# Kernel optimization log

Hardware: AMD Instinct MI355X
Metric: run time of the kernel (lower is better)

Reference implementation:

```python
import jax, jax.numpy as jnp
import numpy as np

NEG_INF = -1e38


def _wkv_scan(time_decay, time_first, key, value):
    # key, value: [B, S, D]; time_decay/time_first: [D]
    B, S, D = key.shape
    w = -jnp.exp(time_decay)  # decay applied additively in log-space

    def step(carry, kv):
        num, den, mx = carry
        k, v = kv  # [B, D]
        # output with current token boosted by time_first
        m_out = jnp.maximum(mx, k + time_first)
        e1 = jnp.exp(mx - m_out)
        e2 = jnp.exp(k + time_first - m_out)
        out = (e1 * num + e2 * v) / (e1 * den + e2)
        # state update with decay
        m_new = jnp.maximum(mx + w, k)
        e1 = jnp.exp(mx + w - m_new)
        e2 = jnp.exp(k - m_new)
        return (e1 * num + e2 * v, e1 * den + e2, m_new), out

    init = (jnp.zeros((B, D), jnp.float32),
            jnp.zeros((B, D), jnp.float32),
            jnp.full((B, D), NEG_INF, jnp.float32))
    kv = (jnp.moveaxis(key, 1, 0), jnp.moveaxis(value, 1, 0))  # [S, B, D]
    _, out = jax.lax.scan(step, init, kv)
    return jnp.moveaxis(out, 0, 1)  # [B, S, D]


def setup_inputs() -> dict:
    key = jax.random.key(0)
    ks = jax.random.split(key, 10)
    B, S, H = 4, 2048, 2048
    D = H  # attention_hidden_size
    return {
        "hidden": jax.random.normal(ks[0], (B, S, H), jnp.float32),
        "time_decay": jax.random.normal(ks[1], (D,), jnp.float32),
        "time_first": jax.random.normal(ks[2], (D,), jnp.float32),
        "time_mix_key": jax.random.uniform(ks[3], (1, 1, H), jnp.float32),
        "time_mix_value": jax.random.uniform(ks[4], (1, 1, H), jnp.float32),
        "time_mix_receptance": jax.random.uniform(ks[5], (1, 1, H), jnp.float32),
        "Wk": jax.random.normal(ks[6], (D, H), jnp.float32) / np.sqrt(H),  # torch Linear weight [out, in]
        "Wv": jax.random.normal(ks[7], (D, H), jnp.float32) / np.sqrt(H),
        "Wr": jax.random.normal(ks[8], (D, H), jnp.float32) / np.sqrt(H),
        "Wo": jax.random.normal(ks[9], (H, D), jnp.float32) / np.sqrt(D),
    }


def reference(hidden, time_decay, time_first, time_mix_key, time_mix_value,
              time_mix_receptance, Wk, Wv, Wr, Wo):
    # time_shift: prepend a zero timestep, drop the last (ZeroPad2d((0,0,1,-1)))
    shifted = jnp.pad(hidden, ((0, 0), (1, 0), (0, 0)))[:, :-1]
    xk = hidden * time_mix_key + shifted * (1.0 - time_mix_key)
    xv = hidden * time_mix_value + shifted * (1.0 - time_mix_value)
    xr = hidden * time_mix_receptance + shifted * (1.0 - time_mix_receptance)
    k = jnp.einsum('bsh,dh->bsd', xk, Wk)
    v = jnp.einsum('bsh,dh->bsd', xv, Wv)
    r = jax.nn.sigmoid(jnp.einsum('bsh,dh->bsd', xr, Wr))
    rwkv = _wkv_scan(time_decay, time_first, k, v)
    return jnp.einsum('bsd,hd->bsh', r * rwkv, Wo)
```

## Files before the change

### kernel.cpp

```cpp
#include <hip/hip_runtime.h>


typedef __attribute__((ext_vector_type(8))) short s16x8;
typedef __attribute__((ext_vector_type(16))) float f32x16;

__device__ __forceinline__ unsigned short f2bf(float f) {
  union { float f; unsigned u; } v; v.f = f;
  unsigned r = v.u + 0x7fffu + ((v.u >> 16) & 1u);
  return (unsigned short)(r >> 16);
}
__device__ __forceinline__ float bf2f(unsigned short h) {
  union { unsigned u; float f; } v; v.u = ((unsigned)h) << 16; return v.f;
}
__device__ __forceinline__ void gload_lds16(const void* g, void* l) {
  __builtin_amdgcn_global_load_lds(
      (const __attribute__((address_space(1))) void*)g,
      (__attribute__((address_space(3))) void*)l, 16, 0, 0);
}


__global__ void conv_bf16(const float4* __restrict__ src, ushort4* __restrict__ dst, int n4) {
  int i = blockIdx.x * blockDim.x + threadIdx.x;
  if (i >= n4) return;
  float4 v = src[i];
  ushort4 o;
  o.x = f2bf(v.x); o.y = f2bf(v.y); o.z = f2bf(v.z); o.w = f2bf(v.w);
  dst[i] = o;
}


__global__ void prep_mix3(const float4* __restrict__ hidden,
                          const float4* __restrict__ tmk,
                          const float4* __restrict__ tmv,
                          const float4* __restrict__ tmr,
                          ushort4* __restrict__ xk, ushort4* __restrict__ xv,
                          ushort4* __restrict__ xr,
                          int S, int H4, long long total4) {
  long long i = (long long)blockIdx.x * blockDim.x + threadIdx.x;
  if (i >= total4) return;
  int h4 = (int)(i % H4);
  long long sb = i / H4;
  int s = (int)(sb % S);
  float4 cur = hidden[i];
  float4 prev = make_float4(0.f, 0.f, 0.f, 0.f);
  if (s > 0) prev = hidden[i - H4];
  float4 mk = tmk[h4], mv = tmv[h4], mr = tmr[h4];
  ushort4 ok, ov, orr;
  ok.x = f2bf(cur.x * mk.x + prev.x * (1.f - mk.x));
  ok.y = f2bf(cur.y * mk.y + prev.y * (1.f - mk.y));
  ok.z = f2bf(cur.z * mk.z + prev.z * (1.f - mk.z));
  ok.w = f2bf(cur.w * mk.w + prev.w * (1.f - mk.w));
  ov.x = f2bf(cur.x * mv.x + prev.x * (1.f - mv.x));
  ov.y = f2bf(cur.y * mv.y + prev.y * (1.f - mv.y));
  ov.z = f2bf(cur.z * mv.z + prev.z * (1.f - mv.z));
  ov.w = f2bf(cur.w * mv.w + prev.w * (1.f - mv.w));
  orr.x = f2bf(cur.x * mr.x + prev.x * (1.f - mr.x));
  orr.y = f2bf(cur.y * mr.y + prev.y * (1.f - mr.y));
  orr.z = f2bf(cur.z * mr.z + prev.z * (1.f - mr.z));
  orr.w = f2bf(cur.w * mr.w + prev.w * (1.f - mr.w));
  xk[i] = ok; xv[i] = ov; xr[i] = orr;
}


#define TM 128
#define TN 128
#define TK 32

template <int EPI>
__global__ __launch_bounds__(256) void gemm_bt(
    const unsigned short* __restrict__ A, const unsigned short* __restrict__ B,
    float* __restrict__ Cf, unsigned short* __restrict__ Cb,
    int M, int N, int K) {
  __shared__ unsigned short lA[2][TM * TK];
  __shared__ unsigned short lB[2][TN * TK];

  const int tid = threadIdx.x;
  const int wave = tid >> 6;
  const int lane = tid & 63;
  const int bm = blockIdx.x * TM;
  const int bn = blockIdx.y * TN;
  const int wm = (wave >> 1) * 64;
  const int wn = (wave & 1) * 64;
  const int lrow = lane & 31;
  const int lq = lane >> 5;

  f32x16 acc[2][2] = {};

  const int st_row0 = wave * 16 + (lane >> 2);
  const int st_row1 = (wave + 4) * 16 + (lane >> 2);
  const int st_c0 = (lane & 3) ^ ((st_row0 >> 1) & 3);
  const int st_c1 = (lane & 3) ^ ((st_row1 >> 1) & 3);
  const unsigned short* pA0 = A + (long long)(bm + st_row0) * K + st_c0 * 8;
  const unsigned short* pA1 = A + (long long)(bm + st_row1) * K + st_c1 * 8;
  const unsigned short* pB0 = B + (long long)(bn + st_row0) * K + st_c0 * 8;
  const unsigned short* pB1 = B + (long long)(bn + st_row1) * K + st_c1 * 8;

  int offA[2][2], offB[2][2];
#pragma unroll
  for (int t = 0; t < 2; ++t)
#pragma unroll
    for (int h = 0; h < 2; ++h) {
      int ar = wm + t * 32 + lrow;
      int br = wn + t * 32 + lrow;
      int c = h * 2 + lq;
      offA[t][h] = ar * TK + ((c ^ ((ar >> 1) & 3)) * 8);
      offB[t][h] = br * TK + ((c ^ ((br >> 1) & 3)) * 8);
    }

  gload_lds16(pA0, &lA[0][wave * 512]);
  gload_lds16(pA1, &lA[0][(wave + 4) * 512]);
  gload_lds16(pB0, &lB[0][wave * 512]);
  gload_lds16(pB1, &lB[0][(wave + 4) * 512]);
  pA0 += TK; pA1 += TK; pB0 += TK; pB1 += TK;

  int p = 0;
  for (int k0 = 0; k0 < K; k0 += TK) {
    __syncthreads();
    if (k0 + TK < K) {
      gload_lds16(pA0, &lA[p ^ 1][wave * 512]);
      gload_lds16(pA1, &lA[p ^ 1][(wave + 4) * 512]);
      gload_lds16(pB0, &lB[p ^ 1][wave * 512]);
      gload_lds16(pB1, &lB[p ^ 1][(wave + 4) * 512]);
      pA0 += TK; pA1 += TK; pB0 += TK; pB1 += TK;
    }

    s16x8 af[2][2], bfr[2][2];
#pragma unroll
    for (int t = 0; t < 2; ++t)
#pragma unroll
      for (int h = 0; h < 2; ++h) {
        af[t][h]  = *(const s16x8*)&lA[p][offA[t][h]];
        bfr[t][h] = *(const s16x8*)&lB[p][offB[t][h]];
      }
#pragma unroll
    for (int h = 0; h < 2; ++h)
#pragma unroll
      for (int mt = 0; mt < 2; ++mt)
#pragma unroll
        for (int nt = 0; nt < 2; ++nt)
          acc[mt][nt] = __builtin_amdgcn_mfma_f32_32x32x16_bf16(
              af[mt][h], bfr[nt][h], acc[mt][nt], 0, 0, 0);
    p ^= 1;
  }

#pragma unroll
  for (int mt = 0; mt < 2; ++mt)
#pragma unroll
    for (int nt = 0; nt < 2; ++nt)
#pragma unroll
      for (int r = 0; r < 16; ++r) {
        int row = bm + wm + mt * 32 + (r & 3) + 8 * (r >> 2) + 4 * lq;
        int col = bn + wn + nt * 32 + lrow;
        float v = acc[mt][nt][r];
        long long idx = (long long)row * N + col;
        if (EPI == 0) {
          Cf[idx] = v;
        } else if (EPI == 1) {
          float s = 1.f / (1.f + __expf(-v));
          Cb[idx] = f2bf(s);
        } else {
          Cb[idx] = f2bf(v);
        }
      }
}


#define NEG_INF_F (-1e38f)

__global__ void scan_phase1(const unsigned short* __restrict__ kb,
                            const unsigned short* __restrict__ vb,
                            const float* __restrict__ td,
                            float* __restrict__ locN, float* __restrict__ locD,
                            float* __restrict__ locM,
                            int S, int D, int C, int L) {
  int t = blockIdx.x * blockDim.x + threadIdx.x;
  int d = t % D;
  int c = (t / D) % C;
  int b = t / (D * C);
  float w = -__expf(td[d]);
  float num = 0.f, den = 0.f, m = NEG_INF_F;
  long long base = ((long long)(b * S + c * L)) * D + d;
  for (int i = 0; i < L; ++i) {
    float kk = bf2f(kb[base]);
    float vv = bf2f(vb[base]);
    base += D;
    float mn = fmaxf(m + w, kk);
    float e1 = __expf(m + w - mn);
    float e2 = __expf(kk - mn);
    num = e1 * num + e2 * vv;
    den = e1 * den + e2;
    m = mn;
  }
  int o = (b * C + c) * D + d;
  locN[o] = num; locD[o] = den; locM[o] = m;
}

__global__ void scan_phase2(const float* __restrict__ td,
                            const float* __restrict__ locN, const float* __restrict__ locD,
                            const float* __restrict__ locM,
                            float* __restrict__ inN, float* __restrict__ inD,
                            float* __restrict__ inM,
                            int Bc, int D, int C, int L) {
  int t = blockIdx.x * blockDim.x + threadIdx.x;
  if (t >= Bc * D) return;
  int d = t % D, b = t / D;
  float w = -__expf(td[d]);
  float Lw = (float)L * w;
  float num = 0.f, den = 0.f, m = NEG_INF_F;
  for (int c = 0; c < C; ++c) {
    int o = (b * C + c) * D + d;
    inN[o] = num; inD[o] = den; inM[o] = m;
    float sm = m + Lw;
    float lm = locM[o];
    float m2 = fmaxf(sm, lm);
    float e1 = __expf(sm - m2);
    float e2 = __expf(lm - m2);
    num = e1 * num + e2 * locN[o];
    den = e1 * den + e2 * locD[o];
    m = m2;
  }
}

__global__ void scan_phase3(const unsigned short* __restrict__ kb,
                            const unsigned short* __restrict__ vb,
                            const unsigned short* __restrict__ rb,
                            const float* __restrict__ td, const float* __restrict__ tfirst,
                            const float* __restrict__ inN, const float* __restrict__ inD,
                            const float* __restrict__ inM,
                            unsigned short* __restrict__ rr,
                            int S, int D, int C, int L) {
  int t = blockIdx.x * blockDim.x + threadIdx.x;
  int d = t % D;
  int c = (t / D) % C;
  int b = t / (D * C);
  float w = -__expf(td[d]);
  float tfd = tfirst[d];
  int o = (b * C + c) * D + d;
  float num = inN[o], den = inD[o], m = inM[o];
  long long base = ((long long)(b * S + c * L)) * D + d;
  for (int i = 0; i < L; ++i) {
    float kk = bf2f(kb[base]);
    float vv = bf2f(vb[base]);
    float rv = bf2f(rb[base]);
    float ktf = kk + tfd;
    float mo = fmaxf(m, ktf);
    float e1 = __expf(m - mo);
    float e2 = __expf(ktf - mo);
    float out = (e1 * num + e2 * vv) / (e1 * den + e2);
    rr[base] = f2bf(out * rv);
    float mn = fmaxf(m + w, kk);
    e1 = __expf(m + w - mn);
    e2 = __expf(kk - mn);
    num = e1 * num + e2 * vv;
    den = e1 * den + e2;
    m = mn;
    base += D;
  }
}


extern "C" void kernel_launch(void* const* d_in, const int* in_sizes, int n_in,
                              void* d_out, int out_size, void* d_ws, size_t ws_size,
                              hipStream_t stream) {
  const float* hidden = (const float*)d_in[0];
  const float* td  = (const float*)d_in[1];
  const float* tfi = (const float*)d_in[2];
  const float* tmk = (const float*)d_in[3];
  const float* tmv = (const float*)d_in[4];
  const float* tmr = (const float*)d_in[5];
  const float* Wk  = (const float*)d_in[6];
  const float* Wv  = (const float*)d_in[7];
  const float* Wr  = (const float*)d_in[8];
  const float* Wo  = (const float*)d_in[9];
  float* out = (float*)d_out;

  const int H = in_sizes[1];
  const int D = H;
  const long long BS = (long long)in_sizes[0] / H;
  const int S = 2048;
  const int B = (int)(BS / S);
  const int C = 32, L = S / C;

  char* ws = (char*)d_ws;
  const size_t MB = 1u << 20;
  unsigned short* W_b = (unsigned short*)(ws + 0 * MB);
  unsigned short* X   = (unsigned short*)(ws + 8 * MB);
  unsigned short* Y   = (unsigned short*)(ws + 40 * MB);
  unsigned short* Z   = (unsigned short*)(ws + 72 * MB);
  float* locN         = (float*)(ws + 104 * MB);
  float* locD         = (float*)(ws + 105 * MB);
  float* locM         = (float*)(ws + 106 * MB);
  float* inN          = (float*)(ws + 107 * MB);
  float* inD          = (float*)(ws + 108 * MB);
  float* inM          = (float*)(ws + 109 * MB);
  unsigned short* kb  = (unsigned short*)out;

  int n4w = H * H / 4;
  int cbk = (n4w + 255) / 256;
  long long total4 = BS * H / 4;
  int pbk = (int)((total4 + 255) / 256);
  dim3 g((unsigned)(BS / TM), (unsigned)(D / TN));

  prep_mix3<<<pbk, 256, 0, stream>>>((const float4*)hidden,
                                     (const float4*)tmk, (const float4*)tmv, (const float4*)tmr,
                                     (ushort4*)X, (ushort4*)Y, (ushort4*)Z, S, H / 4, total4);

  conv_bf16<<<cbk, 256, 0, stream>>>((const float4*)Wk, (ushort4*)W_b, n4w);
  gemm_bt<2><<<g, 256, 0, stream>>>(X, W_b, nullptr, kb, (int)BS, D, H);

  conv_bf16<<<cbk, 256, 0, stream>>>((const float4*)Wv, (ushort4*)W_b, n4w);
  gemm_bt<2><<<g, 256, 0, stream>>>(Y, W_b, nullptr, X, (int)BS, D, H);

  conv_bf16<<<cbk, 256, 0, stream>>>((const float4*)Wr, (ushort4*)W_b, n4w);
  gemm_bt<1><<<g, 256, 0, stream>>>(Z, W_b, nullptr, Y, (int)BS, D, H);

  int nscan = B * C * D;
  scan_phase1<<<nscan / 256, 256, 0, stream>>>(kb, X, td, locN, locD, locM, S, D, C, L);
  scan_phase2<<<(B * D + 255) / 256, 256, 0, stream>>>(td, locN, locD, locM, inN, inD, inM, B, D, C, L);
  scan_phase3<<<nscan / 256, 256, 0, stream>>>(kb, X, Y, td, tfi, inN, inD, inM, Z, S, D, C, L);

  conv_bf16<<<cbk, 256, 0, stream>>>((const float4*)Wo, (ushort4*)W_b, n4w);
  gemm_bt<0><<<g, 256, 0, stream>>>(Z, W_b, out, nullptr, (int)BS, H, D);
}
```

Baseline: 644.1 us.

## Enlarge GEMM tiles to 256x256 with 4-stage LDS pipeline and XCD-aware block remap

Rewrites the bf16 GEMM to use 256x256 output tiles computed by 512 threads, each wave owning a 128x64 sub-tile. Global-to-LDS loads run three stages ahead through a four-buffer ring, with explicit vmcnt waits and barriers replacing double buffering. Blocks are remapped so consecutive IDs spread across the eight XCDs, and MFMA sections raise wave priority. The goal is more data reuse per LDS load and better latency hiding, in exchange for 128KB of LDS per block, more registers, and fewer blocks (256) to fill the GPU.

```diff
diff --git a/kernel.cpp b/kernel.cpp
--- a/kernel.cpp
+++ b/kernel.cpp
@@ -62,89 +62,117 @@
 }
 
 
-#define TM 128
-#define TN 128
-#define TK 32
-
 template <int EPI>
-__global__ __launch_bounds__(256) void gemm_bt(
+__global__ __launch_bounds__(512) void gemm_bt(
     const unsigned short* __restrict__ A, const unsigned short* __restrict__ B,
     float* __restrict__ Cf, unsigned short* __restrict__ Cb,
     int M, int N, int K) {
-  __shared__ unsigned short lA[2][TM * TK];
-  __shared__ unsigned short lB[2][TN * TK];
+  __shared__ unsigned short lds[4][16384];
 
   const int tid = threadIdx.x;
   const int wave = tid >> 6;
   const int lane = tid & 63;
-  const int bm = blockIdx.x * TM;
-  const int bn = blockIdx.y * TN;
-  const int wm = (wave >> 1) * 64;
-  const int wn = (wave & 1) * 64;
+
+  const int nwg = (int)gridDim.x;
+  const int q = nwg >> 3;
+  const int wg = (blockIdx.x & 7) * q + (blockIdx.x >> 3);
+  const int GM = M >> 8;
+  const int bm = (wg % GM) * 256;
+  const int bn = (wg / GM) * 256;
+
+  const int wm = (wave >> 2) * 128;
+  const int wn = (wave & 3) * 64;
   const int lrow = lane & 31;
   const int lq = lane >> 5;
 
-  f32x16 acc[2][2] = {};
-
-  const int st_row0 = wave * 16 + (lane >> 2);
-  const int st_row1 = (wave + 4) * 16 + (lane >> 2);
-  const int st_c0 = (lane & 3) ^ ((st_row0 >> 1) & 3);
-  const int st_c1 = (lane & 3) ^ ((st_row1 >> 1) & 3);
-  const unsigned short* pA0 = A + (long long)(bm + st_row0) * K + st_c0 * 8;
-  const unsigned short* pA1 = A + (long long)(bm + st_row1) * K + st_c1 * 8;
-  const unsigned short* pB0 = B + (long long)(bn + st_row0) * K + st_c0 * 8;
-  const unsigned short* pB1 = B + (long long)(bn + st_row1) * K + st_c1 * 8;
-
-  int offA[2][2], offB[2][2];
-#pragma unroll
-  for (int t = 0; t < 2; ++t)
+  f32x16 acc[4][2] = {};
+
+  const int srow = tid >> 2;
+  const int sg = ((tid & 3) ^ ((srow >> 1) & 3)) * 8;
+  const unsigned short* gA0 = A + (long long)(bm + srow) * K + sg;
+  const unsigned short* gA1 = A + (long long)(bm + 128 + srow) * K + sg;
+  const unsigned short* gB0 = B + (long long)(bn + srow) * K + sg;
+  const unsigned short* gB1 = B + (long long)(bn + 128 + srow) * K + sg;
+
+#define STAGE(sl)                                              \
+  {                                                            \
+    unsigned short* dst = &lds[sl][0] + wave * 512;            \
+    gload_lds16(gA0, dst);                                     \
+    gload_lds16(gA1, dst + 4096);                              \
+    gload_lds16(gB0, dst + 8192);                              \
+    gload_lds16(gB1, dst + 12288);                             \
+    gA0 += 32; gA1 += 32; gB0 += 32; gB1 += 32;                \
+  }
+
+  int offA[4][2], offB[2][2];
+#pragma unroll
+  for (int mt = 0; mt < 4; ++mt)
 #pragma unroll
     for (int h = 0; h < 2; ++h) {
-      int ar = wm + t * 32 + lrow;
-      int br = wn + t * 32 + lrow;
+      int R = wm + mt * 32 + lrow;
       int c = h * 2 + lq;
-      offA[t][h] = ar * TK + ((c ^ ((ar >> 1) & 3)) * 8);
-      offB[t][h] = br * TK + ((c ^ ((br >> 1) & 3)) * 8);
+      offA[mt][h] = R * 32 + ((c ^ ((R >> 1) & 3)) * 8);
     }
-
-  gload_lds16(pA0, &lA[0][wave * 512]);
-  gload_lds16(pA1, &lA[0][(wave + 4) * 512]);
-  gload_lds16(pB0, &lB[0][wave * 512]);
-  gload_lds16(pB1, &lB[0][(wave + 4) * 512]);
-  pA0 += TK; pA1 += TK; pB0 += TK; pB1 += TK;
-
-  int p = 0;
-  for (int k0 = 0; k0 < K; k0 += TK) {
-    __syncthreads();
-    if (k0 + TK < K) {
-      gload_lds16(pA0, &lA[p ^ 1][wave * 512]);
-      gload_lds16(pA1, &lA[p ^ 1][(wave + 4) * 512]);
-      gload_lds16(pB0, &lB[p ^ 1][wave * 512]);
-      gload_lds16(pB1, &lB[p ^ 1][(wave + 4) * 512]);
-      pA0 += TK; pA1 += TK; pB0 += TK; pB1 += TK;
+#pragma unroll
+  for (int nt = 0; nt < 2; ++nt)
+#pragma unroll
+    for (int h = 0; h < 2; ++h) {
+      int Cc = wn + nt * 32 + lrow;
+      int c = h * 2 + lq;
+      offB[nt][h] = 8192 + Cc * 32 + ((c ^ ((Cc >> 1) & 3)) * 8);
     }
 
-    s16x8 af[2][2], bfr[2][2];
-#pragma unroll
-    for (int t = 0; t < 2; ++t)
-#pragma unroll
-      for (int h = 0; h < 2; ++h) {
-        af[t][h]  = *(const s16x8*)&lA[p][offA[t][h]];
-        bfr[t][h] = *(const s16x8*)&lB[p][offB[t][h]];
-      }
+  const int NT = K >> 5;
+
+  STAGE(0);
+  STAGE(1);
+  STAGE(2);
+  asm volatile("s_waitcnt vmcnt(8)" ::: "memory");
+  __builtin_amdgcn_sched_barrier(0);
+  __builtin_amdgcn_s_barrier();
+
+  for (int t = 0; t < NT; ++t) {
+    const unsigned short* sb = &lds[t & 3][0];
+    s16x8 af[4][2], bfr[2][2];
+#pragma unroll
+    for (int mt = 0; mt < 4; ++mt)
+#pragma unroll
+      for (int h = 0; h < 2; ++h)
+        af[mt][h] = *(const s16x8*)(sb + offA[mt][h]);
+#pragma unroll
+    for (int nt = 0; nt < 2; ++nt)
+#pragma unroll
+      for (int h = 0; h < 2; ++h)
+        bfr[nt][h] = *(const s16x8*)(sb + offB[nt][h]);
+
+    if (t + 3 < NT) STAGE((t + 3) & 3);
+
+    if (t + 3 < NT) {
+      asm volatile("s_waitcnt vmcnt(8)" ::: "memory");
+    } else if (t + 3 == NT) {
+      asm volatile("s_waitcnt vmcnt(4)" ::: "memory");
+    } else if (t + 2 == NT) {
+      asm volatile("s_waitcnt vmcnt(0)" ::: "memory");
+    }
+    __builtin_amdgcn_sched_barrier(0);
+    __builtin_amdgcn_s_barrier();
+
+    __builtin_amdgcn_s_setprio(1);
 #pragma unroll
     for (int h = 0; h < 2; ++h)
 #pragma unroll
-      for (int mt = 0; mt < 2; ++mt)
+      for (int mt = 0; mt < 4; ++mt)
 #pragma unroll
         for (int nt = 0; nt < 2; ++nt)
           acc[mt][nt] = __builtin_amdgcn_mfma_f32_32x32x16_bf16(
               af[mt][h], bfr[nt][h], acc[mt][nt], 0, 0, 0);
-    p ^= 1;
-  }
-
-#pragma unroll
-  for (int mt = 0; mt < 2; ++mt)
+    __builtin_amdgcn_s_setprio(0);
+    __builtin_amdgcn_s_barrier();
+  }
+#undef STAGE
+
+#pragma unroll
+  for (int mt = 0; mt < 4; ++mt)
 #pragma unroll
     for (int nt = 0; nt < 2; ++nt)
 #pragma unroll
@@ -299,20 +327,20 @@
   int cbk = (n4w + 255) / 256;
   long long total4 = BS * H / 4;
   int pbk = (int)((total4 + 255) / 256);
-  dim3 g((unsigned)(BS / TM), (unsigned)(D / TN));
+  int nwg = (int)((BS / 256) * (D / 256));
 
   prep_mix3<<<pbk, 256, 0, stream>>>((const float4*)hidden,
                                      (const float4*)tmk, (const float4*)tmv, (const float4*)tmr,
                                      (ushort4*)X, (ushort4*)Y, (ushort4*)Z, S, H / 4, total4);
 
   conv_bf16<<<cbk, 256, 0, stream>>>((const float4*)Wk, (ushort4*)W_b, n4w);
-  gemm_bt<2><<<g, 256, 0, stream>>>(X, W_b, nullptr, kb, (int)BS, D, H);
+  gemm_bt<2><<<nwg, 512, 0, stream>>>(X, W_b, nullptr, kb, (int)BS, D, H);
 
   conv_bf16<<<cbk, 256, 0, stream>>>((const float4*)Wv, (ushort4*)W_b, n4w);
-  gemm_bt<2><<<g, 256, 0, stream>>>(Y, W_b, nullptr, X, (int)BS, D, H);
+  gemm_bt<2><<<nwg, 512, 0, stream>>>(Y, W_b, nullptr, X, (int)BS, D, H);
 
   conv_bf16<<<cbk, 256, 0, stream>>>((const float4*)Wr, (ushort4*)W_b, n4w);
-  gemm_bt<1><<<g, 256, 0, stream>>>(Z, W_b, nullptr, Y, (int)BS, D, H);
+  gemm_bt<1><<<nwg, 512, 0, stream>>>(Z, W_b, nullptr, Y, (int)BS, D, H);
 
   int nscan = B * C * D;
   scan_phase1<<<nscan / 256, 256, 0, stream>>>(kb, X, td, locN, locD, locM, S, D, C, L);
@@ -320,5 +348,5 @@
   scan_phase3<<<nscan / 256, 256, 0, stream>>>(kb, X, Y, td, tfi, inN, inD, inM, Z, S, D, C, L);
 
   conv_bf16<<<cbk, 256, 0, stream>>>((const float4*)Wo, (ushort4*)W_b, n4w);
-  gemm_bt<0><<<g, 256, 0, stream>>>(Z, W_b, out, nullptr, (int)BS, H, D);
-}
+  gemm_bt<0><<<nwg, 512, 0, stream>>>(Z, W_b, out, nullptr, (int)BS, H, D);
+}
```

Result: faster. 558.2 us (-13.3%).
